# Optimization experiments

Hardware: AMD Instinct MI355X
Metric: run time of the kernel (lower is better)

Reference implementation:

```python
import jax, jax.numpy as jnp
import numpy as np

B, S, H = 8, 1024, 16
DV = 1024      # video_input_dim
LAT = 1024     # latent_dim
DQ = LAT // H  # query_dim = 64
DH = 64        # head_dim


def setup_inputs() -> dict:
    key = jax.random.key(0)
    ks = jax.random.split(key, 12)
    sc = lambda fan_in: 1.0 / np.sqrt(fan_in)
    return {
        "input": jax.random.normal(ks[0], (B, S, DV), jnp.float32),
        "latent": jax.random.normal(ks[1], (B, S, LAT), jnp.float32),
        "attention_mask": jax.random.randint(ks[2], (B * H, S, S), 0, 2, jnp.int32),
        "Wq": jax.random.normal(ks[3], (LAT, H * DQ), jnp.float32) * sc(LAT),
        "bq": jnp.zeros((H * DQ,), jnp.float32),
        "Wk": jax.random.normal(ks[4], (DV, H * DQ), jnp.float32) * sc(DV),
        "bk": jnp.zeros((H * DQ,), jnp.float32),
        "Wv": jax.random.normal(ks[5], (DV, H * DH), jnp.float32) * sc(DV),
        "bv": jnp.zeros((H * DH,), jnp.float32),
        "Wo": jax.random.normal(ks[6], (H * DH, LAT), jnp.float32) * sc(H * DH),
        "bo": jnp.zeros((LAT,), jnp.float32),
    }


def reference(input, latent, attention_mask, Wq, bq, Wk, bk, Wv, bv, Wo, bo):
    b, s, _ = input.shape
    # projections -> [b, h, s, d]
    q = (latent @ Wq + bq).reshape(b, s, H, DQ).transpose(0, 2, 1, 3)
    k = (input @ Wk + bk).reshape(b, s, H, DQ).transpose(0, 2, 1, 3)
    v = (input @ Wv + bv).reshape(b, s, H, DH).transpose(0, 2, 1, 3)
    # [b, h, s, s] score matrix (materialized, as in the original bmm)
    scores = jnp.einsum("bhqd,bhkd->bhqk", q, k) / jnp.sqrt(jnp.float32(DQ))
    mask = attention_mask.reshape(b, H, s, s)
    scores = jnp.where(mask == 0, -jnp.inf, scores)
    weights = jax.nn.softmax(scores, axis=-1)
    out = jnp.einsum("bhqk,bhkd->bhqd", weights, v)  # [b, h, s, dh]
    out = out.transpose(0, 2, 1, 3).reshape(b, s, H * DH)
    return out @ Wo + bo
```

## Files before the change

kernel.cpp:

```cpp
#include <hip/hip_runtime.h>
#include <hip/hip_bf16.h>
#include <stdint.h>

typedef __bf16 bf16;
typedef __bf16 bf16x8 __attribute__((ext_vector_type(8)));
typedef float f32x4 __attribute__((ext_vector_type(4)));
typedef unsigned short u16;
typedef unsigned short u16x4 __attribute__((ext_vector_type(4)));


__device__ __forceinline__ void gld16(const bf16* g, bf16* l) {
    __builtin_amdgcn_global_load_lds(
        (const __attribute__((address_space(1))) void*)g,
        (__attribute__((address_space(3))) void*)l, 16, 0, 0);
}

__global__ void convert_f32_bf16(const float* __restrict__ s0, bf16* __restrict__ d0,
                                 const float* __restrict__ s1, bf16* __restrict__ d1) {
    const float* src = blockIdx.y ? s1 : s0;
    bf16* dst = blockIdx.y ? d1 : d0;
    const int nchunk = (8 * 1024 * 1024) / 4;
    for (int c = blockIdx.x * blockDim.x + threadIdx.x; c < nchunk;
         c += gridDim.x * blockDim.x) {
        float4 v = *(const float4*)&src[(size_t)c * 4];
        u16x4 o;
        o[0] = __builtin_bit_cast(u16, (bf16)v.x);
        o[1] = __builtin_bit_cast(u16, (bf16)v.y);
        o[2] = __builtin_bit_cast(u16, (bf16)v.z);
        o[3] = __builtin_bit_cast(u16, (bf16)v.w);
        *(u16x4*)&dst[(size_t)c * 4] = o;
    }
}

__global__ void transpose4(const float* __restrict__ w0, const float* __restrict__ w1,
                           const float* __restrict__ w2, const float* __restrict__ w3,
                           bf16* __restrict__ t0, bf16* __restrict__ t1,
                           bf16* __restrict__ t2, bf16* __restrict__ t3) {
    __shared__ float tile[32][33];
    const float* src; bf16* dst;
    switch (blockIdx.z) {
        case 0:  src = w0; dst = t0; break;
        case 1:  src = w1; dst = t1; break;
        case 2:  src = w2; dst = t2; break;
        default: src = w3; dst = t3; break;
    }
    int tx = threadIdx.x, ty = threadIdx.y;
    int x = blockIdx.x * 32 + tx;
    int y = blockIdx.y * 32 + ty;
    #pragma unroll
    for (int j = 0; j < 32; j += 8)
        tile[ty + j][tx] = src[(size_t)(y + j) * 1024 + x];
    __syncthreads();
    int x2 = blockIdx.y * 32 + tx;
    int y2 = blockIdx.x * 32 + ty;
    #pragma unroll
    for (int j = 0; j < 32; j += 8)
        dst[(size_t)(y2 + j) * 1024 + x2] = (bf16)tile[tx][ty + j];
}

template<int MODE>
__global__ __launch_bounds__(256) void gemm_bt(const bf16* __restrict__ X,
                                               const bf16* __restrict__ Wt,
                                               const float* __restrict__ bias,
                                               void* __restrict__ outv) {
    __shared__ bf16 Al[128 * 32];
    __shared__ bf16 Bl[128 * 32];
    const int tid  = threadIdx.x;
    const int m0   = blockIdx.x * 128;
    const int n0   = blockIdx.y * 128;
    const int lane = tid & 63;
    const int w    = tid >> 6;
    const int wm   = (w & 1) * 64;
    const int wn   = (w >> 1) * 64;
    const int l15  = lane & 15;
    const int quad = lane >> 4;
    const int sw   = (l15 >> 1) & 3;

    f32x4 acc[4][4] = {};

    for (int kt = 0; kt < 1024; kt += 32) {
        __syncthreads();
        #pragma unroll
        for (int t = 0; t < 2; t++) {
            int c = (w * 2 + t) * 64 + lane;
            int row = c >> 2;
            int e   = (c & 3) ^ ((c >> 3) & 3);
            gld16(&X [(size_t)(m0 + row) * 1024 + kt + e * 8], &Al[(w * 2 + t) * 512]);
            gld16(&Wt[(size_t)(n0 + row) * 1024 + kt + e * 8], &Bl[(w * 2 + t) * 512]);
        }
        __syncthreads();
        bf16x8 a[4], b[4];
        #pragma unroll
        for (int i = 0; i < 4; i++)
            a[i] = *(const bf16x8*)&Al[(wm + i * 16 + l15) * 32 + (quad ^ sw) * 8];
        #pragma unroll
        for (int j = 0; j < 4; j++)
            b[j] = *(const bf16x8*)&Bl[(wn + j * 16 + l15) * 32 + (quad ^ sw) * 8];
        #pragma unroll
        for (int i = 0; i < 4; i++)
            #pragma unroll
            for (int j = 0; j < 4; j++)
                acc[i][j] = __builtin_amdgcn_mfma_f32_16x16x32_bf16(a[i], b[j], acc[i][j], 0, 0, 0);
    }

    float bv[4];
    #pragma unroll
    for (int j = 0; j < 4; j++) bv[j] = bias[n0 + wn + j * 16 + l15];

    #pragma unroll
    for (int i = 0; i < 4; i++) {
        int mbase = m0 + wm + i * 16 + quad * 4;
        #pragma unroll
        for (int j = 0; j < 4; j++) {
            int n = n0 + wn + j * 16 + l15;
            if (MODE == 2) {
                bf16* out = (bf16*)outv;
                int b = mbase >> 10, s = mbase & 1023;
                int h = n >> 6, d = n & 63;
                u16x4 pack;
                #pragma unroll
                for (int r = 0; r < 4; r++) {
                    bf16 v = (bf16)(acc[i][j][r] + bv[j]);
                    pack[r] = __builtin_bit_cast(u16, v);
                }
                *(u16x4*)&out[(((size_t)(b * 16 + h)) * 64 + d) * 1024 + s] = pack;
            } else if (MODE == 1) {
                bf16* out = (bf16*)outv;
                #pragma unroll
                for (int r = 0; r < 4; r++) {
                    int m = mbase + r;
                    int b = m >> 10, s = m & 1023;
                    int h = n >> 6, d = n & 63;
                    out[(((size_t)(b * 16 + h)) * 1024 + s) * 64 + d] =
                        (bf16)(acc[i][j][r] + bv[j]);
                }
            } else {
                float* out = (float*)outv;
                #pragma unroll
                for (int r = 0; r < 4; r++)
                    out[(size_t)(mbase + r) * 1024 + n] = acc[i][j][r] + bv[j];
            }
        }
    }
}

__global__ __launch_bounds__(256, 2) void attn(const bf16* __restrict__ Q,
                                               const bf16* __restrict__ K,
                                               const bf16* __restrict__ Vt,
                                               const int*  __restrict__ mask,
                                               bf16* __restrict__ O) {
    __shared__ bf16 Kl[2][4096];
    __shared__ bf16 Vl[2][4096];
    __shared__ bf16 Pl[4][32 * 68];

    const int tid  = threadIdx.x;
    const int lane = tid & 63;
    const int w    = tid >> 6;
    const int l15  = lane & 15;
    const int quad = lane >> 4;

    const int blk = blockIdx.x;
    const int bh  = (blk & 7) * 16 + (blk >> 6);
    const int q0  = ((blk >> 3) & 7) * 128;
    const int qrow0 = q0 + w * 32;

    const bf16* Kbh = K  + (size_t)bh * 65536;
    const bf16* Vbh = Vt + (size_t)bh * 65536;
    const int* mbase = mask + ((size_t)bh * 1024 + qrow0 + quad * 4) * 1024;

    bf16x8 qa[2][2];
    #pragma unroll
    for (int rb = 0; rb < 2; rb++) {
        const bf16* Qb = Q + ((size_t)bh * 1024 + qrow0 + rb * 16 + l15) * 64;
        qa[rb][0] = *(const bf16x8*)&Qb[quad * 8];
        qa[rb][1] = *(const bf16x8*)&Qb[32 + quad * 8];
    }

    const int c0 = (w * 2 + 0) * 64 + lane;
    const int c1 = (w * 2 + 1) * 64 + lane;
    const int swz = l15 & 7;

    #define STAGE_KV(kk, buf)                                                          \
        {                                                                              \
            int r0 = c0 >> 3, e0 = (c0 & 7) ^ (r0 & 7);                                \
            int r1 = c1 >> 3, e1 = (c1 & 7) ^ (r1 & 7);                                \
            gld16(&Kbh[(size_t)((kk) + r0) * 64 + e0 * 8], &Kl[buf][(w * 2 + 0) * 512]); \
            gld16(&Kbh[(size_t)((kk) + r1) * 64 + e1 * 8], &Kl[buf][(w * 2 + 1) * 512]); \
            gld16(&Vbh[(size_t)r0 * 1024 + (kk) + e0 * 8], &Vl[buf][(w * 2 + 0) * 512]); \
            gld16(&Vbh[(size_t)r1 * 1024 + (kk) + e1 * 8], &Vl[buf][(w * 2 + 1) * 512]); \
        }

    STAGE_KV(0, 0);
    int mn[2][4][4];
    #pragma unroll
    for (int rb = 0; rb < 2; rb++)
        #pragma unroll
        for (int r = 0; r < 4; r++)
            #pragma unroll
            for (int t = 0; t < 4; t++)
                mn[rb][r][t] = mbase[(size_t)(rb * 16 + r) * 1024 + t * 16 + l15];

    f32x4 o[2][4] = {};
    float lsum[2][4] = {};
    bf16* Pw = Pl[w];

    for (int it = 0; it < 16; it++) {
        __syncthreads();
        const int cur = it & 1, nxt = cur ^ 1;
        const int kn = ((it + 1) & 15) * 64;

        int nib[2][4];
        #pragma unroll
        for (int rb = 0; rb < 2; rb++)
            #pragma unroll
            for (int r = 0; r < 4; r++)
                nib[rb][r] = (mn[rb][r][0] != 0) | ((mn[rb][r][1] != 0) << 1) |
                             ((mn[rb][r][2] != 0) << 2) | ((mn[rb][r][3] != 0) << 3);

        STAGE_KV(kn, nxt);
        #pragma unroll
        for (int rb = 0; rb < 2; rb++)
            #pragma unroll
            for (int r = 0; r < 4; r++)
                #pragma unroll
                for (int t = 0; t < 4; t++)
                    mn[rb][r][t] = mbase[(size_t)(rb * 16 + r) * 1024 + kn + t * 16 + l15];

        f32x4 s[2][4];
        #pragma unroll
        for (int t = 0; t < 4; t++) {
            bf16x8 kb0 = *(const bf16x8*)&Kl[cur][(t * 16 + l15) * 64 + ((0 + quad) ^ swz) * 8];
            bf16x8 kb1 = *(const bf16x8*)&Kl[cur][(t * 16 + l15) * 64 + ((4 + quad) ^ swz) * 8];
            #pragma unroll
            for (int rb = 0; rb < 2; rb++) {
                f32x4 z = {};
                z = __builtin_amdgcn_mfma_f32_16x16x32_bf16(qa[rb][0], kb0, z, 0, 0, 0);
                z = __builtin_amdgcn_mfma_f32_16x16x32_bf16(qa[rb][1], kb1, z, 0, 0, 0);
                s[rb][t] = z;
            }
        }

        #pragma unroll
        for (int rb = 0; rb < 2; rb++)
            #pragma unroll
            for (int t = 0; t < 4; t++)
                #pragma unroll
                for (int r = 0; r < 4; r++) {
                    float p = __expf(fmaf(s[rb][t][r], 0.125f, -12.0f));
                    p = ((nib[rb][r] >> t) & 1) ? p : 0.0f;
                    lsum[rb][r] += p;
                    Pw[(rb * 16 + quad * 4 + r) * 68 + t * 16 + l15] = (bf16)p;
                }

        bf16x8 pa[2][2];
        #pragma unroll
        for (int rb = 0; rb < 2; rb++) {
            pa[rb][0] = *(const bf16x8*)&Pw[(rb * 16 + l15) * 68 + quad * 8];
            pa[rb][1] = *(const bf16x8*)&Pw[(rb * 16 + l15) * 68 + 32 + quad * 8];
        }
        #pragma unroll
        for (int nt = 0; nt < 4; nt++) {
            bf16x8 vb0 = *(const bf16x8*)&Vl[cur][(nt * 16 + l15) * 64 + ((0 + quad) ^ swz) * 8];
            bf16x8 vb1 = *(const bf16x8*)&Vl[cur][(nt * 16 + l15) * 64 + ((4 + quad) ^ swz) * 8];
            #pragma unroll
            for (int rb = 0; rb < 2; rb++) {
                o[rb][nt] = __builtin_amdgcn_mfma_f32_16x16x32_bf16(pa[rb][0], vb0, o[rb][nt], 0, 0, 0);
                o[rb][nt] = __builtin_amdgcn_mfma_f32_16x16x32_bf16(pa[rb][1], vb1, o[rb][nt], 0, 0, 0);
            }
        }
    }
    #undef STAGE_KV

    const int b = bh >> 4, h = bh & 15;
    #pragma unroll
    for (int rb = 0; rb < 2; rb++)
        #pragma unroll
        for (int r = 0; r < 4; r++) {
            float l = lsum[rb][r];
            #pragma unroll
            for (int off = 1; off < 16; off <<= 1)
                l += __shfl_xor(l, off, 64);
            float inv = 1.0f / l;
            int srow = qrow0 + rb * 16 + quad * 4 + r;
            bf16* orow = O + ((size_t)(b * 1024 + srow)) * 1024 + h * 64;
            #pragma unroll
            for (int nt = 0; nt < 4; nt++)
                orow[nt * 16 + l15] = (bf16)(o[rb][nt][r] * inv);
        }
}

extern "C" void kernel_launch(void* const* d_in, const int* in_sizes, int n_in,
                              void* d_out, int out_size, void* d_ws, size_t ws_size,
                              hipStream_t stream) {
    const float* input  = (const float*)d_in[0];
    const float* latent = (const float*)d_in[1];
    const int*   mask   = (const int*)d_in[2];
    const float* Wq = (const float*)d_in[3];
    const float* bq = (const float*)d_in[4];
    const float* Wk = (const float*)d_in[5];
    const float* bk = (const float*)d_in[6];
    const float* Wv = (const float*)d_in[7];
    const float* bv = (const float*)d_in[8];
    const float* Wo = (const float*)d_in[9];
    const float* bo = (const float*)d_in[10];
    float* out = (float*)d_out;

    char* ws = (char*)d_ws;
    bf16* Xb  = (bf16*)(ws);
    bf16* Lb  = (bf16*)(ws + (16u << 20));
    bf16* Qh  = (bf16*)(ws + (32u << 20));
    bf16* Kh  = (bf16*)(ws + (48u << 20));
    bf16* Vt  = (bf16*)(ws + (64u << 20));
    bf16* Ob  = (bf16*)(ws + (80u << 20));
    bf16* Wqt = (bf16*)(ws + (96u << 20));
    bf16* Wkt = (bf16*)(ws + (98u << 20));
    bf16* Wvt = (bf16*)(ws + (100u << 20));
    bf16* Wot = (bf16*)(ws + (102u << 20));

    convert_f32_bf16<<<dim3(2048, 2, 1), 256, 0, stream>>>(input, Xb, latent, Lb);

    transpose4<<<dim3(32, 32, 4), dim3(32, 8, 1), 0, stream>>>(
        Wq, Wk, Wv, Wo, Wqt, Wkt, Wvt, Wot);

    dim3 g(64, 8, 1);
    gemm_bt<1><<<g, 256, 0, stream>>>(Lb, Wqt, bq, Qh);
    gemm_bt<1><<<g, 256, 0, stream>>>(Xb, Wkt, bk, Kh);
    gemm_bt<2><<<g, 256, 0, stream>>>(Xb, Wvt, bv, Vt);

    attn<<<dim3(1024, 1, 1), 256, 0, stream>>>(Qh, Kh, Vt, mask, Ob);

    gemm_bt<0><<<g, 256, 0, stream>>>(Ob, Wot, bo, out);
}
```

Measured before the change: 918.8 us.

## Merge prep kernels and QKV GEMMs into single launches, raise occupancy hints

The f32->bf16 conversion and weight transpose kernels are merged into one prep launch, and the three Q/K/V projection GEMMs become one launch with blockIdx.z selecting the operands. The GEMM and attention kernels now request 3 blocks per SIMD instead of the default or 2. This cuts launch count and lets the three projections fill the GPU together (1536 blocks), at the cost of runtime mode branching and possible register pressure or spills under the tighter launch bounds.

```diff
diff --git a/kernel.cpp b/kernel.cpp
--- a/kernel.cpp
+++ b/kernel.cpp
@@ -15,59 +15,61 @@
         (__attribute__((address_space(3))) void*)l, 16, 0, 0);
 }
 
-__global__ void convert_f32_bf16(const float* __restrict__ s0, bf16* __restrict__ d0,
-                                 const float* __restrict__ s1, bf16* __restrict__ d1) {
-    const float* src = blockIdx.y ? s1 : s0;
-    bf16* dst = blockIdx.y ? d1 : d0;
-    const int nchunk = (8 * 1024 * 1024) / 4;
-    for (int c = blockIdx.x * blockDim.x + threadIdx.x; c < nchunk;
-         c += gridDim.x * blockDim.x) {
-        float4 v = *(const float4*)&src[(size_t)c * 4];
-        u16x4 o;
-        o[0] = __builtin_bit_cast(u16, (bf16)v.x);
-        o[1] = __builtin_bit_cast(u16, (bf16)v.y);
-        o[2] = __builtin_bit_cast(u16, (bf16)v.z);
-        o[3] = __builtin_bit_cast(u16, (bf16)v.w);
-        *(u16x4*)&dst[(size_t)c * 4] = o;
-    }
-}
-
-__global__ void transpose4(const float* __restrict__ w0, const float* __restrict__ w1,
-                           const float* __restrict__ w2, const float* __restrict__ w3,
-                           bf16* __restrict__ t0, bf16* __restrict__ t1,
-                           bf16* __restrict__ t2, bf16* __restrict__ t3) {
+__global__ __launch_bounds__(256) void prep(
+        const float* __restrict__ input, const float* __restrict__ latent,
+        bf16* __restrict__ Xb, bf16* __restrict__ Lb,
+        const float* __restrict__ w0, const float* __restrict__ w1,
+        const float* __restrict__ w2, const float* __restrict__ w3,
+        bf16* __restrict__ t0, bf16* __restrict__ t1,
+        bf16* __restrict__ t2, bf16* __restrict__ t3) {
     __shared__ float tile[32][33];
-    const float* src; bf16* dst;
-    switch (blockIdx.z) {
-        case 0:  src = w0; dst = t0; break;
-        case 1:  src = w1; dst = t1; break;
-        case 2:  src = w2; dst = t2; break;
-        default: src = w3; dst = t3; break;
-    }
-    int tx = threadIdx.x, ty = threadIdx.y;
-    int x = blockIdx.x * 32 + tx;
-    int y = blockIdx.y * 32 + ty;
-    #pragma unroll
-    for (int j = 0; j < 32; j += 8)
-        tile[ty + j][tx] = src[(size_t)(y + j) * 1024 + x];
-    __syncthreads();
-    int x2 = blockIdx.y * 32 + tx;
-    int y2 = blockIdx.x * 32 + ty;
-    #pragma unroll
-    for (int j = 0; j < 32; j += 8)
-        dst[(size_t)(y2 + j) * 1024 + x2] = (bf16)tile[tx][ty + j];
-}
-
-template<int MODE>
-__global__ __launch_bounds__(256) void gemm_bt(const bf16* __restrict__ X,
-                                               const bf16* __restrict__ Wt,
-                                               const float* __restrict__ bias,
-                                               void* __restrict__ outv) {
-    __shared__ bf16 Al[128 * 32];
-    __shared__ bf16 Bl[128 * 32];
+    const int bid = blockIdx.x;
+    const int tid = threadIdx.x;
+    if (bid < 4096) {
+        const float* src = (bid >> 11) ? latent : input;
+        bf16* dst = (bid >> 11) ? Lb : Xb;
+        const int nchunk = (8 * 1024 * 1024) / 4;
+        for (int c = (bid & 2047) * 256 + tid; c < nchunk; c += 2048 * 256) {
+            float4 v = *(const float4*)&src[(size_t)c * 4];
+            u16x4 o;
+            o[0] = __builtin_bit_cast(u16, (bf16)v.x);
+            o[1] = __builtin_bit_cast(u16, (bf16)v.y);
+            o[2] = __builtin_bit_cast(u16, (bf16)v.z);
+            o[3] = __builtin_bit_cast(u16, (bf16)v.w);
+            *(u16x4*)&dst[(size_t)c * 4] = o;
+        }
+    } else {
+        const int tb = bid - 4096;
+        const float* src; bf16* dst;
+        switch (tb >> 10) {
+            case 0:  src = w0; dst = t0; break;
+            case 1:  src = w1; dst = t1; break;
+            case 2:  src = w2; dst = t2; break;
+            default: src = w3; dst = t3; break;
+        }
+        const int r  = tb & 1023;
+        const int bx = r & 31, by = r >> 5;
+        const int tx = tid & 31, ty = tid >> 5;
+        const int x = bx * 32 + tx;
+        const int y = by * 32 + ty;
+        #pragma unroll
+        for (int j = 0; j < 32; j += 8)
+            tile[ty + j][tx] = src[(size_t)(y + j) * 1024 + x];
+        __syncthreads();
+        const int x2 = by * 32 + tx;
+        const int y2 = bx * 32 + ty;
+        #pragma unroll
+        for (int j = 0; j < 32; j += 8)
+            dst[(size_t)(y2 + j) * 1024 + x2] = (bf16)tile[tx][ty + j];
+    }
+}
+
+__device__ __forceinline__ void gemm_core(const bf16* __restrict__ X,
+                                          const bf16* __restrict__ Wt,
+                                          const float* __restrict__ bias,
+                                          void* __restrict__ outv, int mode,
+                                          int m0, int n0, bf16* Al, bf16* Bl) {
     const int tid  = threadIdx.x;
-    const int m0   = blockIdx.x * 128;
-    const int n0   = blockIdx.y * 128;
     const int lane = tid & 63;
     const int w    = tid >> 6;
     const int wm   = (w & 1) * 64;
@@ -113,7 +115,7 @@
         #pragma unroll
         for (int j = 0; j < 4; j++) {
             int n = n0 + wn + j * 16 + l15;
-            if (MODE == 2) {
+            if (mode == 2) {
                 bf16* out = (bf16*)outv;
                 int b = mbase >> 10, s = mbase & 1023;
                 int h = n >> 6, d = n & 63;
@@ -124,7 +126,7 @@
                     pack[r] = __builtin_bit_cast(u16, v);
                 }
                 *(u16x4*)&out[(((size_t)(b * 16 + h)) * 64 + d) * 1024 + s] = pack;
-            } else if (MODE == 1) {
+            } else if (mode == 1) {
                 bf16* out = (bf16*)outv;
                 #pragma unroll
                 for (int r = 0; r < 4; r++) {
@@ -144,7 +146,33 @@
     }
 }
 
-__global__ __launch_bounds__(256, 2) void attn(const bf16* __restrict__ Q,
+__global__ __launch_bounds__(256, 3) void gemm_qkv(
+        const bf16* __restrict__ Lb, const bf16* __restrict__ Xb,
+        const bf16* __restrict__ Wqt, const bf16* __restrict__ Wkt,
+        const bf16* __restrict__ Wvt,
+        const float* __restrict__ bq, const float* __restrict__ bk,
+        const float* __restrict__ bv,
+        bf16* __restrict__ Qh, bf16* __restrict__ Kh, bf16* __restrict__ Vt) {
+    __shared__ bf16 Al[128 * 32];
+    __shared__ bf16 Bl[128 * 32];
+    const bf16* X; const bf16* Wt; const float* bias; void* out; int mode;
+    switch (blockIdx.z) {
+        case 0:  X = Lb; Wt = Wqt; bias = bq; out = Qh; mode = 1; break;
+        case 1:  X = Xb; Wt = Wkt; bias = bk; out = Kh; mode = 1; break;
+        default: X = Xb; Wt = Wvt; bias = bv; out = Vt; mode = 2; break;
+    }
+    gemm_core(X, Wt, bias, out, mode, blockIdx.x * 128, blockIdx.y * 128, Al, Bl);
+}
+
+__global__ __launch_bounds__(256, 3) void gemm_o(
+        const bf16* __restrict__ Ob, const bf16* __restrict__ Wot,
+        const float* __restrict__ bo, float* __restrict__ out) {
+    __shared__ bf16 Al[128 * 32];
+    __shared__ bf16 Bl[128 * 32];
+    gemm_core(Ob, Wot, bo, out, 0, blockIdx.x * 128, blockIdx.y * 128, Al, Bl);
+}
+
+__global__ __launch_bounds__(256, 3) void attn(const bf16* __restrict__ Q,
                                                const bf16* __restrict__ K,
                                                const bf16* __restrict__ Vt,
                                                const int*  __restrict__ mask,
@@ -317,17 +345,13 @@
     bf16* Wvt = (bf16*)(ws + (100u << 20));
     bf16* Wot = (bf16*)(ws + (102u << 20));
 
-    convert_f32_bf16<<<dim3(2048, 2, 1), 256, 0, stream>>>(input, Xb, latent, Lb);
-
-    transpose4<<<dim3(32, 32, 4), dim3(32, 8, 1), 0, stream>>>(
-        Wq, Wk, Wv, Wo, Wqt, Wkt, Wvt, Wot);
-
-    dim3 g(64, 8, 1);
-    gemm_bt<1><<<g, 256, 0, stream>>>(Lb, Wqt, bq, Qh);
-    gemm_bt<1><<<g, 256, 0, stream>>>(Xb, Wkt, bk, Kh);
-    gemm_bt<2><<<g, 256, 0, stream>>>(Xb, Wvt, bv, Vt);
+    prep<<<dim3(8192, 1, 1), 256, 0, stream>>>(
+        input, latent, Xb, Lb, Wq, Wk, Wv, Wo, Wqt, Wkt, Wvt, Wot);
+
+    gemm_qkv<<<dim3(64, 8, 3), 256, 0, stream>>>(
+        Lb, Xb, Wqt, Wkt, Wvt, bq, bk, bv, Qh, Kh, Vt);
 
     attn<<<dim3(1024, 1, 1), 256, 0, stream>>>(Qh, Kh, Vt, mask, Ob);
 
-    gemm_bt<0><<<g, 256, 0, stream>>>(Ob, Wot, bo, out);
-}
+    gemm_o<<<dim3(64, 8, 1), 256, 0, stream>>>(Ob, Wot, bo, out);
+}
```

Result: no change. 935.3 us (+1.8%).
